# Performance work log

Measured on AMD Instinct MI355X. Metric: run time of the kernel, lower is better.

The kernel has to match this reference:

```python
import jax, jax.numpy as jnp
import numpy as np

N_HEADS, N_LEVELS, N_POINTS = 8, 3, 4


def _bilinear_sample(valf, Hl, Wl, grid):
    """torch.F.grid_sample(mode='bilinear', padding_mode='zeros', align_corners=False).
    valf: [B, nH, hd, Hl*Wl] flattened per-head value map
    grid: [B, Q, nH, P, 2] normalized (x, y) in [-1, 1]
    returns [B, nH, hd, Q, P]
    """
    B, Q, nH, P, _ = grid.shape
    hd = valf.shape[2]
    # unnormalize (align_corners=False)
    ix = ((grid[..., 0] + 1.0) * Wl - 1.0) * 0.5  # [B,Q,nH,P]
    iy = ((grid[..., 1] + 1.0) * Hl - 1.0) * 0.5
    x0 = jnp.floor(ix); y0 = jnp.floor(iy)
    x1 = x0 + 1.0;      y1 = y0 + 1.0
    # corner weights
    w00 = (x1 - ix) * (y1 - iy)
    w01 = (ix - x0) * (y1 - iy)
    w10 = (x1 - ix) * (iy - y0)
    w11 = (ix - x0) * (iy - y0)

    def gather(xi, yi):
        inb = (xi >= 0) & (xi <= Wl - 1) & (yi >= 0) & (yi <= Hl - 1)  # zero padding
        xc = jnp.clip(xi, 0, Wl - 1).astype(jnp.int32)
        yc = jnp.clip(yi, 0, Hl - 1).astype(jnp.int32)
        idx = yc * Wl + xc                              # [B,Q,nH,P]
        idx = idx.transpose(0, 2, 1, 3).reshape(B, nH, 1, Q * P)
        idx = jnp.broadcast_to(idx, (B, nH, hd, Q * P))
        g = jnp.take_along_axis(valf, idx, axis=3)      # [B,nH,hd,Q*P]
        g = g.reshape(B, nH, hd, Q, P)
        mask = inb.transpose(0, 2, 1, 3)[:, :, None, :, :]
        return g * mask

    def w_(w):  # [B,Q,nH,P] -> [B,nH,1,Q,P]
        return w.transpose(0, 2, 1, 3)[:, :, None, :, :]

    return (gather(x0, y0) * w_(w00) + gather(x1, y0) * w_(w01)
            + gather(x0, y1) * w_(w10) + gather(x1, y1) * w_(w11))


def _deform_attn(query, feats, reference_points,
                 W_off, b_off, W_attn, b_attn, W_val, b_val, W_out, b_out):
    B, Q, D = query.shape
    nH, L, P = N_HEADS, N_LEVELS, N_POINTS
    hd = D // nH
    # sampling offsets: tanh * 0.5
    off = jnp.tanh(query @ W_off + b_off).reshape(B, Q, nH, L, P, 2) * 0.5
    # attention weights: softmax over levels*points
    aw = jax.nn.softmax((query @ W_attn + b_attn).reshape(B, Q, nH, L * P), axis=-1)
    aw = aw.reshape(B, Q, nH, L, P)

    out = jnp.zeros((B, Q, nH, hd), dtype=query.dtype)
    for lvl, feat in enumerate(feats):
        Hl, Wl = feat.shape[2], feat.shape[3]
        # value projection on flattened map
        v = feat.reshape(B, D, Hl * Wl).transpose(0, 2, 1) @ W_val + b_val  # [B,S,D]
        valf = v.reshape(B, Hl * Wl, nH, hd).transpose(0, 2, 3, 1)          # [B,nH,hd,S]
        grid = (reference_points[:, :, None, None, :] + off[:, :, :, lvl]) * 2.0 - 1.0  # [B,Q,nH,P,2]
        sampled = _bilinear_sample(valf, Hl, Wl, grid)                      # [B,nH,hd,Q,P]
        w = aw[:, :, :, lvl].transpose(0, 2, 1, 3)[:, :, None, :, :]        # [B,nH,1,Q,P]
        out = out + (sampled * w).sum(-1).transpose(0, 3, 1, 2)             # [B,Q,nH,hd]
    return out.reshape(B, Q, D) @ W_out + b_out


def setup_inputs() -> dict:
    key = jax.random.key(0)
    ks = jax.random.split(key, 13)
    B, Q, D = 4, 8400, 256
    return {
        "query": jax.random.normal(ks[0], (B, Q, D), jnp.float32),
        "feat0": jax.random.normal(ks[1], (B, D, 80, 80), jnp.float32),
        "feat1": jax.random.normal(ks[2], (B, D, 40, 40), jnp.float32),
        "feat2": jax.random.normal(ks[3], (B, D, 20, 20), jnp.float32),
        "reference_points": jax.random.uniform(ks[4], (B, Q, 2), jnp.float32),
        "W_off": jax.random.normal(ks[5], (D, N_HEADS * N_LEVELS * N_POINTS * 2), jnp.float32) * 0.02,
        "b_off": jax.random.normal(ks[6], (N_HEADS * N_LEVELS * N_POINTS * 2,), jnp.float32) * 0.02,
        "W_attn": jax.random.normal(ks[7], (D, N_HEADS * N_LEVELS * N_POINTS), jnp.float32) * 0.02,
        "b_attn": jax.random.normal(ks[8], (N_HEADS * N_LEVELS * N_POINTS,), jnp.float32) * 0.02,
        "W_val": jax.random.normal(ks[9], (D, D), jnp.float32) * (1.0 / np.sqrt(D)),
        "b_val": jnp.zeros((D,), jnp.float32),
        "W_out": jax.random.normal(ks[10], (D, D), jnp.float32) * (1.0 / np.sqrt(D)),
        "b_out": jnp.zeros((D,), jnp.float32),
    }


def reference(query, feat0, feat1, feat2, reference_points,
              W_off, b_off, W_attn, b_attn, W_val, b_val, W_out, b_out):
    return _deform_attn(query, [feat0, feat1, feat2], reference_points,
                        W_off, b_off, W_attn, b_attn, W_val, b_val, W_out, b_out)
```

## Files before the change

kernel.cpp:

```cpp
#include <hip/hip_runtime.h>
#include <math.h>

#define NH    8
#define DIM   256
#define NQ    8400
#define BATCH 4
#define STOT  8400
#define MQ    (BATCH * NQ)

typedef _Float16 f16;
typedef __attribute__((ext_vector_type(8))) _Float16 f16x8;
typedef __attribute__((ext_vector_type(8))) unsigned short u16x8;
typedef __attribute__((ext_vector_type(4))) float  f32x4;

__global__ __launch_bounds__(256) void prep_w(
    const float* __restrict__ W_val, const float* __restrict__ W_out,
    const float* __restrict__ W_off, const float* __restrict__ W_attn,
    const float* __restrict__ b_off, const float* __restrict__ b_attn,
    f16* __restrict__ Wvt, f16* __restrict__ Wot, f16* __restrict__ Wch,
    float* __restrict__ bcat)
{
    const int z = blockIdx.z;
    const int t = threadIdx.x;
    if (z == 4) {
        if (blockIdx.x == 0 && blockIdx.y == 0)
            for (int i = t; i < 288; i += 256)
                bcat[i] = (i < 192) ? b_off[i] : b_attn[i - 192];
        return;
    }
    const float* W; f16* oH; int Nw, n0;
    switch (z) {
        case 0:  W = W_val;  oH = Wvt; Nw = 256; n0 = 0;   break;
        case 1:  W = W_out;  oH = Wot; Nw = 256; n0 = 0;   break;
        case 2:  W = W_off;  oH = Wch; Nw = 192; n0 = 0;   break;
        default: W = W_attn; oH = Wch; Nw = 96;  n0 = 192; break;
    }
    const int nb = blockIdx.x * 32, k0 = blockIdx.y * 32;
    if (nb >= Nw) return;
    __shared__ float tile[32][33];
    const int c = t & 31, r = t >> 5;
    #pragma unroll
    for (int i = 0; i < 4; ++i) {
        int k = k0 + r + i * 8, n = nb + c;
        tile[r + i * 8][c] = (n < Nw) ? W[(size_t)k * Nw + n] : 0.f;
    }
    __syncthreads();
    #pragma unroll
    for (int i = 0; i < 4; ++i) {
        int n = nb + r + i * 8, k = k0 + c;
        if (n < Nw)
            oH[(size_t)(n0 + n) * 256 + k] = (f16)tile[c][r + i * 8];
    }
}

__global__ __launch_bounds__(256) void prep_af(
    const float* __restrict__ feat0, const float* __restrict__ feat1,
    const float* __restrict__ feat2, const float* __restrict__ query,
    f16* __restrict__ Af, f16* __restrict__ Qh)
{
    const int z = blockIdx.z;
    const int t = threadIdx.x;
    if (z >= 4) {
        int lid = (z - 4) * 263 * 8 + blockIdx.x * 8 + blockIdx.y;
        size_t idx = (size_t)lid * 1024 + t * 4;
        if (idx < (size_t)MQ * 256) {
            float4 q = *(const float4*)(query + idx);
            f16 h0 = (f16)q.x, h1 = (f16)q.y, h2 = (f16)q.z, h3 = (f16)q.w;
            ushort4 hv;
            hv.x = __builtin_bit_cast(unsigned short, h0);
            hv.y = __builtin_bit_cast(unsigned short, h1);
            hv.z = __builtin_bit_cast(unsigned short, h2);
            hv.w = __builtin_bit_cast(unsigned short, h3);
            *(ushort4*)((unsigned short*)Qh + idx) = hv;
        }
        return;
    }
    const int b = z;
    const int s0 = blockIdx.x * 32, k0 = blockIdx.y * 32;
    const float* f0b = feat0 + (size_t)b * 256 * 6400;
    const float* f1b = feat1 + (size_t)b * 256 * 1600;
    const float* f2b = feat2 + (size_t)b * 256 * 400;
    __shared__ float tile[32][33];
    const int c = t & 31, r = t >> 5;
    #pragma unroll
    for (int i = 0; i < 4; ++i) {
        int rr = r + i * 8;
        int s = s0 + c;
        float v = 0.f;
        if (s < 8400) {
            const float* fp; int S, sl;
            if (s < 6400)      { fp = f0b; S = 6400; sl = s; }
            else if (s < 8000) { fp = f1b; S = 1600; sl = s - 6400; }
            else               { fp = f2b; S = 400;  sl = s - 8000; }
            v = fp[(size_t)(k0 + rr) * S + sl];
        }
        tile[rr][c] = v;
    }
    __syncthreads();
    #pragma unroll
    for (int i = 0; i < 4; ++i) {
        int s = s0 + r + i * 8, k = k0 + c;
        if (s < 8400)
            Af[((size_t)b * 8400 + s) * 256 + k] = (f16)tile[c][r + i * 8];
    }
}

__global__ __launch_bounds__(256) void gemm_vr(
    const f16* __restrict__ Af, const f16* __restrict__ Qh,
    const f16* __restrict__ Wvt, const f16* __restrict__ Wch,
    const float* __restrict__ b_val, const float* __restrict__ bcat,
    f16* __restrict__ valh, float* __restrict__ rawo, f16* __restrict__ attnh)
{
    __shared__ unsigned short Ah[128 * 40];
    __shared__ unsigned short Bs[128 * 40];

    const bool split = blockIdx.x >= 2;
    const int bn = split ? (blockIdx.x - 2) * 128 : blockIdx.x * 128;
    const int bm = blockIdx.y * 128;
    const int N = split ? 288 : 256;
    const unsigned short* Ag = (const unsigned short*)(split ? Qh : Af);
    const unsigned short* Bg = (const unsigned short*)(split ? Wch : Wvt);

    const int t = threadIdx.x;
    const int lane = t & 63, w = t >> 6;
    const int wm = (w & 1) * 64, wn = (w >> 1) * 64;
    const int l15 = lane & 15, quad = lane >> 4;

    f32x4 acc[4][4];
    #pragma unroll
    for (int i = 0; i < 4; ++i)
        #pragma unroll
        for (int j = 0; j < 4; ++j)
            acc[i][j] = (f32x4){0.f, 0.f, 0.f, 0.f};

    for (int k0 = 0; k0 < 256; k0 += 32) {
        #pragma unroll
        for (int cc = 0; cc < 2; ++cc) {
            int cid = t + cc * 256;
            int r = cid >> 2, s = cid & 3;
            int gr = bm + r; if (gr > MQ - 1) gr = MQ - 1;
            *(u16x8*)&Ah[r * 40 + s * 8] = *(const u16x8*)(Ag + (size_t)gr * 256 + k0 + s * 8);
            int gn = bn + r; if (gn > N - 1) gn = N - 1;
            *(u16x8*)&Bs[r * 40 + s * 8] = *(const u16x8*)(Bg + (size_t)gn * 256 + k0 + s * 8);
        }
        __syncthreads();

        f16x8 af[4], bfv[4];
        #pragma unroll
        for (int mt = 0; mt < 4; ++mt)
            af[mt] = *(const f16x8*)&Ah[(wm + mt * 16 + l15) * 40 + quad * 8];
        #pragma unroll
        for (int nt = 0; nt < 4; ++nt)
            bfv[nt] = *(const f16x8*)&Bs[(wn + nt * 16 + l15) * 40 + quad * 8];
        #pragma unroll
        for (int mt = 0; mt < 4; ++mt)
            #pragma unroll
            for (int nt = 0; nt < 4; ++nt)
                acc[mt][nt] = __builtin_amdgcn_mfma_f32_16x16x32_f16(af[mt], bfv[nt], acc[mt][nt], 0, 0, 0);
        __syncthreads();
    }

    #pragma unroll
    for (int nt = 0; nt < 4; ++nt) {
        int col = bn + wn + nt * 16 + l15;
        float bv = (col < N) ? (split ? bcat[col] : b_val[col]) : 0.f;
        #pragma unroll
        for (int mt = 0; mt < 4; ++mt) {
            int row0 = bm + wm + mt * 16 + quad * 4;
            #pragma unroll
            for (int r = 0; r < 4; ++r) {
                int row = row0 + r;
                if (row < MQ && col < N) {
                    float v = acc[mt][nt][r] + bv;
                    if (!split) {
                        int bb = row / STOT, s = row - bb * STOT;
                        int h = col >> 5, c = col & 31;
                        valh[(((size_t)(bb * 8 + h)) * STOT + s) * 32 + c] = (f16)v;
                    } else if (col < 192) {
                        rawo[(size_t)row * 192 + col] = v;
                    } else {
                        attnh[(size_t)row * 96 + (col - 192)] = (f16)v;
                    }
                }
            }
        }
    }
}

__global__ __launch_bounds__(256) void gemm_o(
    const f16* __restrict__ A, const f16* __restrict__ Bt,
    const float* __restrict__ bias, float* __restrict__ C)
{
    __shared__ unsigned short Ah[128 * 40];
    __shared__ unsigned short Bs[128 * 40];
    const int t = threadIdx.x;
    const int bn = blockIdx.x * 128, bm = blockIdx.y * 128;
    const int lane = t & 63, w = t >> 6;
    const int wm = (w & 1) * 64, wn = (w >> 1) * 64;
    const int l15 = lane & 15, quad = lane >> 4;

    f32x4 acc[4][4];
    #pragma unroll
    for (int i = 0; i < 4; ++i)
        #pragma unroll
        for (int j = 0; j < 4; ++j)
            acc[i][j] = (f32x4){0.f, 0.f, 0.f, 0.f};

    for (int k0 = 0; k0 < 256; k0 += 32) {
        #pragma unroll
        for (int cc = 0; cc < 2; ++cc) {
            int cid = t + cc * 256;
            int r = cid >> 2, s = cid & 3;
            int gr = bm + r; if (gr > MQ - 1) gr = MQ - 1;
            *(u16x8*)&Ah[r * 40 + s * 8] = *(const u16x8*)((const unsigned short*)A + (size_t)gr * 256 + k0 + s * 8);
            *(u16x8*)&Bs[r * 40 + s * 8] = *(const u16x8*)((const unsigned short*)Bt + (size_t)(bn + r) * 256 + k0 + s * 8);
        }
        __syncthreads();
        f16x8 af[4], bfv[4];
        #pragma unroll
        for (int mt = 0; mt < 4; ++mt)
            af[mt] = *(const f16x8*)&Ah[(wm + mt * 16 + l15) * 40 + quad * 8];
        #pragma unroll
        for (int nt = 0; nt < 4; ++nt)
            bfv[nt] = *(const f16x8*)&Bs[(wn + nt * 16 + l15) * 40 + quad * 8];
        #pragma unroll
        for (int mt = 0; mt < 4; ++mt)
            #pragma unroll
            for (int nt = 0; nt < 4; ++nt)
                acc[mt][nt] = __builtin_amdgcn_mfma_f32_16x16x32_f16(af[mt], bfv[nt], acc[mt][nt], 0, 0, 0);
        __syncthreads();
    }
    #pragma unroll
    for (int nt = 0; nt < 4; ++nt) {
        int col = bn + wn + nt * 16 + l15;
        float bv = bias[col];
        #pragma unroll
        for (int mt = 0; mt < 4; ++mt) {
            int row0 = bm + wm + mt * 16 + quad * 4;
            #pragma unroll
            for (int r = 0; r < 4; ++r) {
                int row = row0 + r;
                if (row < MQ)
                    C[(size_t)row * 256 + col] = acc[mt][nt][r] + bv;
            }
        }
    }
}

__global__ __launch_bounds__(256) void sample_v5(
    const f16* __restrict__ valh,
    const float* __restrict__ raw_off,
    const f16* __restrict__ attnh,
    const float* __restrict__ refp,
    f16* __restrict__ out_h)
{
    const int bx = blockIdx.x;
    const int xcd = bx & 7;
    const int b = xcd >> 1;
    const int qi = (bx >> 3) * 2 + (xcd & 1);
    const int bq0 = b * NQ + qi * 8;
    const int t = threadIdx.x;

    __shared__ int   s_idx[8][96][4];
    __shared__ float s_w[8][96][4];
    __shared__ float s_m[8][8];
    __shared__ float s_inv[8][8];

    if (t < 64) {
        int q = t >> 3, h = t & 7;
        const f16* a = attnh + (size_t)(bq0 + q) * 96 + h * 12;
        float m = (float)a[0];
        #pragma unroll
        for (int j = 1; j < 12; ++j) m = fmaxf(m, (float)a[j]);
        float s = 0.f;
        #pragma unroll
        for (int j = 0; j < 12; ++j) s += expf((float)a[j] - m);
        s_m[q][h] = m;
        s_inv[q][h] = 1.f / s;
    }
    __syncthreads();

    for (int i = t; i < 768; i += 256) {
        int q = i / 96, p = i - q * 96;
        int h = p / 12, lp = p - h * 12, l = lp >> 2;
        const int dims[3]   = {80, 40, 20};
        const int bases_[3] = {0, 6400, 8000};
        int Wl = dims[l], base = bases_[l];
        float logit = (float)attnh[(size_t)(bq0 + q) * 96 + p];
        float aw = expf(logit - s_m[q][h]) * s_inv[q][h];
        size_t ro = (size_t)(bq0 + q) * 192 + h * 24 + lp * 2;
        float rawx = raw_off[ro], rawy = raw_off[ro + 1];
        float rx = refp[(size_t)(bq0 + q) * 2];
        float ry = refp[(size_t)(bq0 + q) * 2 + 1];
        float ix = (rx + tanhf(rawx) * 0.5f) * Wl - 0.5f;
        float iy = (ry + tanhf(rawy) * 0.5f) * Wl - 0.5f;
        float x0f = floorf(ix), y0f = floorf(iy);
        float fx = ix - x0f, fy = iy - y0f;
        int x0 = (int)x0f, y0 = (int)y0f;
        float w00 = (1.f - fx) * (1.f - fy) * aw;
        float w01 = fx * (1.f - fy) * aw;
        float w10 = (1.f - fx) * fy * aw;
        float w11 = fx * fy * aw;
        bool vx0 = (unsigned)x0 < (unsigned)Wl;
        bool vx1 = (unsigned)(x0 + 1) < (unsigned)Wl;
        bool vy0 = (unsigned)y0 < (unsigned)Wl;
        bool vy1 = (unsigned)(y0 + 1) < (unsigned)Wl;
        int row0 = base + y0 * Wl, row1 = row0 + Wl;
        s_idx[q][p][0] = (vx0 && vy0) ? row0 + x0     : 0;  s_w[q][p][0] = (vx0 && vy0) ? w00 : 0.f;
        s_idx[q][p][1] = (vx1 && vy0) ? row0 + x0 + 1 : 0;  s_w[q][p][1] = (vx1 && vy0) ? w01 : 0.f;
        s_idx[q][p][2] = (vx0 && vy1) ? row1 + x0     : 0;  s_w[q][p][2] = (vx0 && vy1) ? w10 : 0.f;
        s_idx[q][p][3] = (vx1 && vy1) ? row1 + x0 + 1 : 0;  s_w[q][p][3] = (vx1 && vy1) ? w11 : 0.f;
    }
    __syncthreads();

    const int q = t >> 5;
    const int h = (t >> 2) & 7;
    const int l4 = t & 3;
    const f16* vb = valh + ((size_t)(b * 8 + h) * STOT) * 32 + l4 * 8;
    const int*   ip = &s_idx[q][h * 12][0];
    const float* wp = &s_w[q][h * 12][0];
    float acc[8] = {};
    #pragma unroll
    for (int pp = 0; pp < 4; ++pp) {
        int   ix[12]; float ww[12]; f16x8 v[12];
        #pragma unroll
        for (int k = 0; k < 12; ++k) { ix[k] = ip[pp * 12 + k]; ww[k] = wp[pp * 12 + k]; }
        #pragma unroll
        for (int k = 0; k < 12; ++k) v[k] = *(const f16x8*)(vb + (size_t)ix[k] * 32);
        #pragma unroll
        for (int k = 0; k < 12; ++k)
            #pragma unroll
            for (int c = 0; c < 8; ++c)
                acc[c] = fmaf(ww[k], (float)v[k][c], acc[c]);
    }
    f16x8 ob;
    #pragma unroll
    for (int c = 0; c < 8; ++c) ob[c] = (f16)acc[c];
    *(f16x8*)(out_h + (size_t)(bq0 + q) * 256 + h * 32 + l4 * 8) = ob;
}

extern "C" void kernel_launch(void* const* d_in, const int* in_sizes, int n_in,
                              void* d_out, int out_size, void* d_ws, size_t ws_size,
                              hipStream_t stream)
{
    const float* query  = (const float*)d_in[0];
    const float* feat0  = (const float*)d_in[1];
    const float* feat1  = (const float*)d_in[2];
    const float* feat2  = (const float*)d_in[3];
    const float* refp   = (const float*)d_in[4];
    const float* W_off  = (const float*)d_in[5];
    const float* b_off  = (const float*)d_in[6];
    const float* W_attn = (const float*)d_in[7];
    const float* b_attn = (const float*)d_in[8];
    const float* W_val  = (const float*)d_in[9];
    const float* b_val  = (const float*)d_in[10];
    const float* W_out  = (const float*)d_in[11];
    const float* b_out  = (const float*)d_in[12];
    float* out = (float*)d_out;

    f16*   valh  = (f16*)d_ws;
    float* rawo  = (float*)(valh + (size_t)MQ * 256);
    f16*   attnh = (f16*)(rawo + (size_t)MQ * 192);
    f16*   Af    = attnh + (size_t)MQ * 96;
    f16*   outh  = Af;
    f16*   Qh    = Af + (size_t)MQ * 256;
    f16*   Wvt   = Qh + (size_t)MQ * 256;
    f16*   Wot   = Wvt + 65536;
    f16*   Wch   = Wot + 65536;
    float* bcat  = (float*)(Wch + 73728);

    dim3 blk(256);

    prep_w<<<dim3(8, 8, 5), blk, 0, stream>>>(W_val, W_out, W_off, W_attn,
                                              b_off, b_attn, Wvt, Wot, Wch, bcat);
    prep_af<<<dim3(263, 8, 8), blk, 0, stream>>>(feat0, feat1, feat2, query, Af, Qh);
    gemm_vr<<<dim3(5, 263), blk, 0, stream>>>(Af, Qh, Wvt, Wch, b_val, bcat,
                                              valh, rawo, attnh);
    sample_v5<<<dim3(MQ / 8), blk, 0, stream>>>(valh, rawo, attnh, refp, outh);
    gemm_o<<<dim3(2, 263), blk, 0, stream>>>(outh, Wot, b_out, out);
}
```

Before: 252.2 us.

## Fuse weight and feature prep, convert query in GEMM, use packed fp16 sampling

Merges the weight-transpose and feature-transpose prep kernels into a single launch. The query fp32 to fp16 pre-conversion pass is dropped; the offset/attention GEMM now loads fp32 query and converts it while staging tiles, which removes a full write and read of the fp16 query buffer. The sampling kernel stores bilinear weights as packed fp16 pairs and accumulates each 12-tap group with packed half2 multiply-adds before folding into fp32. This cuts conversion ALU work, at some cost in accumulation precision.

```diff
diff --git a/kernel.cpp b/kernel.cpp
--- a/kernel.cpp
+++ b/kernel.cpp
@@ -9,79 +9,61 @@
 #define MQ    (BATCH * NQ)
 
 typedef _Float16 f16;
+typedef __attribute__((ext_vector_type(2))) _Float16 f16x2;
 typedef __attribute__((ext_vector_type(8))) _Float16 f16x8;
 typedef __attribute__((ext_vector_type(8))) unsigned short u16x8;
 typedef __attribute__((ext_vector_type(4))) float  f32x4;
 
-__global__ __launch_bounds__(256) void prep_w(
+__global__ __launch_bounds__(256) void prep_all(
+    const float* __restrict__ feat0, const float* __restrict__ feat1,
+    const float* __restrict__ feat2,
     const float* __restrict__ W_val, const float* __restrict__ W_out,
     const float* __restrict__ W_off, const float* __restrict__ W_attn,
     const float* __restrict__ b_off, const float* __restrict__ b_attn,
-    f16* __restrict__ Wvt, f16* __restrict__ Wot, f16* __restrict__ Wch,
-    float* __restrict__ bcat)
+    f16* __restrict__ Af, f16* __restrict__ Wvt, f16* __restrict__ Wot,
+    f16* __restrict__ Wch, float* __restrict__ bcat)
 {
     const int z = blockIdx.z;
     const int t = threadIdx.x;
-    if (z == 4) {
-        if (blockIdx.x == 0 && blockIdx.y == 0)
-            for (int i = t; i < 288; i += 256)
-                bcat[i] = (i < 192) ? b_off[i] : b_attn[i - 192];
-        return;
-    }
-    const float* W; f16* oH; int Nw, n0;
-    switch (z) {
-        case 0:  W = W_val;  oH = Wvt; Nw = 256; n0 = 0;   break;
-        case 1:  W = W_out;  oH = Wot; Nw = 256; n0 = 0;   break;
-        case 2:  W = W_off;  oH = Wch; Nw = 192; n0 = 0;   break;
-        default: W = W_attn; oH = Wch; Nw = 96;  n0 = 192; break;
-    }
-    const int nb = blockIdx.x * 32, k0 = blockIdx.y * 32;
-    if (nb >= Nw) return;
     __shared__ float tile[32][33];
     const int c = t & 31, r = t >> 5;
-    #pragma unroll
-    for (int i = 0; i < 4; ++i) {
-        int k = k0 + r + i * 8, n = nb + c;
-        tile[r + i * 8][c] = (n < Nw) ? W[(size_t)k * Nw + n] : 0.f;
-    }
-    __syncthreads();
-    #pragma unroll
-    for (int i = 0; i < 4; ++i) {
-        int n = nb + r + i * 8, k = k0 + c;
-        if (n < Nw)
-            oH[(size_t)(n0 + n) * 256 + k] = (f16)tile[c][r + i * 8];
-    }
-}
-
-__global__ __launch_bounds__(256) void prep_af(
-    const float* __restrict__ feat0, const float* __restrict__ feat1,
-    const float* __restrict__ feat2, const float* __restrict__ query,
-    f16* __restrict__ Af, f16* __restrict__ Qh)
-{
-    const int z = blockIdx.z;
-    const int t = threadIdx.x;
-    if (z >= 4) {
-        int lid = (z - 4) * 263 * 8 + blockIdx.x * 8 + blockIdx.y;
-        size_t idx = (size_t)lid * 1024 + t * 4;
-        if (idx < (size_t)MQ * 256) {
-            float4 q = *(const float4*)(query + idx);
-            f16 h0 = (f16)q.x, h1 = (f16)q.y, h2 = (f16)q.z, h3 = (f16)q.w;
-            ushort4 hv;
-            hv.x = __builtin_bit_cast(unsigned short, h0);
-            hv.y = __builtin_bit_cast(unsigned short, h1);
-            hv.z = __builtin_bit_cast(unsigned short, h2);
-            hv.w = __builtin_bit_cast(unsigned short, h3);
-            *(ushort4*)((unsigned short*)Qh + idx) = hv;
+
+    if (z == 4) {
+        const int xb = blockIdx.x;
+        if (xb > 25) return;
+        if (xb == 25) {
+            if (blockIdx.y == 0)
+                for (int i = t; i < 288; i += 256)
+                    bcat[i] = (i < 192) ? b_off[i] : b_attn[i - 192];
+            return;
+        }
+        const float* W; f16* oH; int Nw, n0, nb;
+        if (xb < 8)       { W = W_val;  oH = Wvt; Nw = 256; n0 = 0;   nb = xb * 32; }
+        else if (xb < 16) { W = W_out;  oH = Wot; Nw = 256; n0 = 0;   nb = (xb - 8) * 32; }
+        else if (xb < 22) { W = W_off;  oH = Wch; Nw = 192; n0 = 0;   nb = (xb - 16) * 32; }
+        else              { W = W_attn; oH = Wch; Nw = 96;  n0 = 192; nb = (xb - 22) * 32; }
+        const int k0 = blockIdx.y * 32;
+        #pragma unroll
+        for (int i = 0; i < 4; ++i) {
+            int k = k0 + r + i * 8, n = nb + c;
+            tile[r + i * 8][c] = (n < Nw) ? W[(size_t)k * Nw + n] : 0.f;
+        }
+        __syncthreads();
+        #pragma unroll
+        for (int i = 0; i < 4; ++i) {
+            int n = nb + r + i * 8, k = k0 + c;
+            if (n < Nw)
+                oH[(size_t)(n0 + n) * 256 + k] = (f16)tile[c][r + i * 8];
         }
         return;
     }
+
     const int b = z;
     const int s0 = blockIdx.x * 32, k0 = blockIdx.y * 32;
+    if (s0 >= 8400) return;
     const float* f0b = feat0 + (size_t)b * 256 * 6400;
     const float* f1b = feat1 + (size_t)b * 256 * 1600;
     const float* f2b = feat2 + (size_t)b * 256 * 400;
-    __shared__ float tile[32][33];
-    const int c = t & 31, r = t >> 5;
     #pragma unroll
     for (int i = 0; i < 4; ++i) {
         int rr = r + i * 8;
@@ -106,7 +88,7 @@
 }
 
 __global__ __launch_bounds__(256) void gemm_vr(
-    const f16* __restrict__ Af, const f16* __restrict__ Qh,
+    const f16* __restrict__ Af, const float* __restrict__ query,
     const f16* __restrict__ Wvt, const f16* __restrict__ Wch,
     const float* __restrict__ b_val, const float* __restrict__ bcat,
     f16* __restrict__ valh, float* __restrict__ rawo, f16* __restrict__ attnh)
@@ -118,7 +100,6 @@
     const int bn = split ? (blockIdx.x - 2) * 128 : blockIdx.x * 128;
     const int bm = blockIdx.y * 128;
     const int N = split ? 288 : 256;
-    const unsigned short* Ag = (const unsigned short*)(split ? Qh : Af);
     const unsigned short* Bg = (const unsigned short*)(split ? Wch : Wvt);
 
     const int t = threadIdx.x;
@@ -139,7 +120,18 @@
             int cid = t + cc * 256;
             int r = cid >> 2, s = cid & 3;
             int gr = bm + r; if (gr > MQ - 1) gr = MQ - 1;
-            *(u16x8*)&Ah[r * 40 + s * 8] = *(const u16x8*)(Ag + (size_t)gr * 256 + k0 + s * 8);
+            if (split) {
+                const float* ap = query + (size_t)gr * 256 + k0 + s * 8;
+                float4 q0 = *(const float4*)ap;
+                float4 q1 = *(const float4*)(ap + 4);
+                f16x8 hv;
+                hv[0] = (f16)q0.x; hv[1] = (f16)q0.y; hv[2] = (f16)q0.z; hv[3] = (f16)q0.w;
+                hv[4] = (f16)q1.x; hv[5] = (f16)q1.y; hv[6] = (f16)q1.z; hv[7] = (f16)q1.w;
+                *(f16x8*)&Ah[r * 40 + s * 8] = hv;
+            } else {
+                *(u16x8*)&Ah[r * 40 + s * 8] =
+                    *(const u16x8*)((const unsigned short*)Af + (size_t)gr * 256 + k0 + s * 8);
+            }
             int gn = bn + r; if (gn > N - 1) gn = N - 1;
             *(u16x8*)&Bs[r * 40 + s * 8] = *(const u16x8*)(Bg + (size_t)gn * 256 + k0 + s * 8);
         }
@@ -247,7 +239,7 @@
     }
 }
 
-__global__ __launch_bounds__(256) void sample_v5(
+__global__ __launch_bounds__(256) void sample_v6(
     const f16* __restrict__ valh,
     const float* __restrict__ raw_off,
     const f16* __restrict__ attnh,
@@ -261,10 +253,10 @@
     const int bq0 = b * NQ + qi * 8;
     const int t = threadIdx.x;
 
-    __shared__ int   s_idx[8][96][4];
-    __shared__ float s_w[8][96][4];
-    __shared__ float s_m[8][8];
-    __shared__ float s_inv[8][8];
+    __shared__ int      s_idx[8][96][4];
+    __shared__ unsigned s_wp[8][96][4];
+    __shared__ float    s_m[8][8];
+    __shared__ float    s_inv[8][8];
 
     if (t < 64) {
         int q = t >> 3, h = t & 7;
@@ -306,36 +298,50 @@
         bool vy0 = (unsigned)y0 < (unsigned)Wl;
         bool vy1 = (unsigned)(y0 + 1) < (unsigned)Wl;
         int row0 = base + y0 * Wl, row1 = row0 + Wl;
-        s_idx[q][p][0] = (vx0 && vy0) ? row0 + x0     : 0;  s_w[q][p][0] = (vx0 && vy0) ? w00 : 0.f;
-        s_idx[q][p][1] = (vx1 && vy0) ? row0 + x0 + 1 : 0;  s_w[q][p][1] = (vx1 && vy0) ? w01 : 0.f;
-        s_idx[q][p][2] = (vx0 && vy1) ? row1 + x0     : 0;  s_w[q][p][2] = (vx0 && vy1) ? w10 : 0.f;
-        s_idx[q][p][3] = (vx1 && vy1) ? row1 + x0 + 1 : 0;  s_w[q][p][3] = (vx1 && vy1) ? w11 : 0.f;
+        float ws[4] = { vx0 && vy0 ? w00 : 0.f, vx1 && vy0 ? w01 : 0.f,
+                        vx0 && vy1 ? w10 : 0.f, vx1 && vy1 ? w11 : 0.f };
+        int   is[4] = { vx0 && vy0 ? row0 + x0 : 0, vx1 && vy0 ? row0 + x0 + 1 : 0,
+                        vx0 && vy1 ? row1 + x0 : 0, vx1 && vy1 ? row1 + x0 + 1 : 0 };
+        #pragma unroll
+        for (int k = 0; k < 4; ++k) {
+            unsigned short us = __builtin_bit_cast(unsigned short, (f16)ws[k]);
+            s_wp[q][p][k] = ((unsigned)us << 16) | us;
+            s_idx[q][p][k] = is[k];
+        }
     }
     __syncthreads();
 
     const int q = t >> 5;
     const int h = (t >> 2) & 7;
     const int l4 = t & 3;
-    const f16* vb = valh + ((size_t)(b * 8 + h) * STOT) * 32 + l4 * 8;
-    const int*   ip = &s_idx[q][h * 12][0];
-    const float* wp = &s_w[q][h * 12][0];
-    float acc[8] = {};
+    const uint4* vb4 = (const uint4*)(valh + (size_t)(b * 8 + h) * STOT * 32);
+    const int*      ip = &s_idx[q][h * 12][0];
+    const unsigned* wp = &s_wp[q][h * 12][0];
+    float accf[8] = {};
     #pragma unroll
     for (int pp = 0; pp < 4; ++pp) {
-        int   ix[12]; float ww[12]; f16x8 v[12];
+        int ix[12]; unsigned ww[12]; uint4 v[12];
         #pragma unroll
         for (int k = 0; k < 12; ++k) { ix[k] = ip[pp * 12 + k]; ww[k] = wp[pp * 12 + k]; }
         #pragma unroll
-        for (int k = 0; k < 12; ++k) v[k] = *(const f16x8*)(vb + (size_t)ix[k] * 32);
-        #pragma unroll
-        for (int k = 0; k < 12; ++k)
-            #pragma unroll
-            for (int c = 0; c < 8; ++c)
-                acc[c] = fmaf(ww[k], (float)v[k][c], acc[c]);
+        for (int k = 0; k < 12; ++k) v[k] = vb4[(size_t)ix[k] * 4 + l4];
+        f16x2 a0 = (f16x2)(f16)0, a1 = a0, a2 = a0, a3 = a0;
+        #pragma unroll
+        for (int k = 0; k < 12; ++k) {
+            f16x2 wv = __builtin_bit_cast(f16x2, ww[k]);
+            a0 += wv * __builtin_bit_cast(f16x2, v[k].x);
+            a1 += wv * __builtin_bit_cast(f16x2, v[k].y);
+            a2 += wv * __builtin_bit_cast(f16x2, v[k].z);
+            a3 += wv * __builtin_bit_cast(f16x2, v[k].w);
+        }
+        accf[0] += (float)a0[0]; accf[1] += (float)a0[1];
+        accf[2] += (float)a1[0]; accf[3] += (float)a1[1];
+        accf[4] += (float)a2[0]; accf[5] += (float)a2[1];
+        accf[6] += (float)a3[0]; accf[7] += (float)a3[1];
     }
     f16x8 ob;
     #pragma unroll
-    for (int c = 0; c < 8; ++c) ob[c] = (f16)acc[c];
+    for (int c = 0; c < 8; ++c) ob[c] = (f16)accf[c];
     *(f16x8*)(out_h + (size_t)(bq0 + q) * 256 + h * 32 + l4 * 8) = ob;
 }
 
@@ -363,19 +369,19 @@
     f16*   attnh = (f16*)(rawo + (size_t)MQ * 192);
     f16*   Af    = attnh + (size_t)MQ * 96;
     f16*   outh  = Af;
-    f16*   Qh    = Af + (size_t)MQ * 256;
-    f16*   Wvt   = Qh + (size_t)MQ * 256;
+    f16*   Wvt   = Af + (size_t)MQ * 256;
     f16*   Wot   = Wvt + 65536;
     f16*   Wch   = Wot + 65536;
     float* bcat  = (float*)(Wch + 73728);
 
     dim3 blk(256);
 
-    prep_w<<<dim3(8, 8, 5), blk, 0, stream>>>(W_val, W_out, W_off, W_attn,
-                                              b_off, b_attn, Wvt, Wot, Wch, bcat);
-    prep_af<<<dim3(263, 8, 8), blk, 0, stream>>>(feat0, feat1, feat2, query, Af, Qh);
-    gemm_vr<<<dim3(5, 263), blk, 0, stream>>>(Af, Qh, Wvt, Wch, b_val, bcat,
+    prep_all<<<dim3(263, 8, 5), blk, 0, stream>>>(feat0, feat1, feat2,
+                                                  W_val, W_out, W_off, W_attn,
+                                                  b_off, b_attn,
+                                                  Af, Wvt, Wot, Wch, bcat);
+    gemm_vr<<<dim3(5, 263), blk, 0, stream>>>(Af, query, Wvt, Wch, b_val, bcat,
                                               valh, rawo, attnh);
-    sample_v5<<<dim3(MQ / 8), blk, 0, stream>>>(valh, rawo, attnh, refp, outh);
+    sample_v6<<<dim3(MQ / 8), blk, 0, stream>>>(valh, rawo, attnh, refp, outh);
     gemm_o<<<dim3(2, 263), blk, 0, stream>>>(outh, Wot, b_out, out);
 }
```

Result: no change. 251.3 us (-0.4%).
